# Optimization experiments

Measured on AMD Instinct MI355X. Metric: run time of the kernel, lower is better.

## Reference

```python
import jax, jax.numpy as jnp
import numpy as np

# db4 reconstruction filters (pywt convention): rec_lo = reversed(dec_lo),
# rec_hi[k] = (-1)^k * dec_lo[k]
REC_LO = [0.23037781330885523, 0.7148465705525415, 0.6308807679295904,
          -0.02798376941698385, -0.18703481171888114, 0.030841381835986965,
          0.032883011666982945, -0.010597401784997278]
REC_HI = [-0.010597401784997278, -0.032883011666982945, 0.030841381835986965,
          0.18703481171888114, -0.02798376941698385, -0.6308807679295904,
          0.7148465705525415, -0.23037781330885523]
FILT_LEN = 8


def _idwt1d(cA, cD, axis):
    """Periodized single-level inverse DWT along `axis`. N -> 2N."""
    cA = jnp.moveaxis(cA, axis, -1)
    cD = jnp.moveaxis(cD, axis, -1)
    N = cA.shape[-1]
    up_a = jnp.zeros(cA.shape[:-1] + (2 * N,), cA.dtype).at[..., ::2].set(cA)
    up_d = jnp.zeros(cD.shape[:-1] + (2 * N,), cD.dtype).at[..., ::2].set(cD)
    # circular synthesis: y[m] = sum_k g[k]*up_a[m-k] + h[k]*up_d[m-k]
    y = sum(REC_LO[k] * jnp.roll(up_a, k, axis=-1) +
            REC_HI[k] * jnp.roll(up_d, k, axis=-1) for k in range(FILT_LEN))
    y = jnp.roll(y, -(FILT_LEN - 2), axis=-1)  # phase alignment (periodization)
    return jnp.moveaxis(y, -1, axis)


def setup_inputs() -> dict:
    key = jax.random.key(0)
    x = jax.random.normal(key, (64, 256, 256, 16), dtype=jnp.float32)
    return {"x": x}


def reference(x):
    # x: [B, H, W, 4*C] with channel groups = (cA, cH, cV, cD)
    c = x.shape[-1] // 4
    cA, cH, cV, cD = (x[..., :c], x[..., c:2 * c],
                      x[..., 2 * c:3 * c], x[..., 3 * c:])
    lo = _idwt1d(cA, cH, axis=1)   # [B, 2H, W, C]
    hi = _idwt1d(cV, cD, axis=1)   # [B, 2H, W, C]
    return _idwt1d(lo, hi, axis=2)  # [B, 2H, 2W, C]
```

## Files before the change

### kernel.cpp

```cpp
#include <hip/hip_runtime.h>
#include <hip/hip_bf16.h>


#define N 256
#define RJ 8

typedef float f32x4 __attribute__((ext_vector_type(4)));

#define LGKM_BARRIER()                                   \
  do {                                                   \
    asm volatile("s_waitcnt lgkmcnt(0)" ::: "memory");   \
    __builtin_amdgcn_s_barrier();                        \
    asm volatile("" ::: "memory");                       \
  } while (0)

__device__ __forceinline__ f32x4 fma4v(const f32x4 acc, const float s,
                                       const f32x4 a) {
  const f32x4 sv = {s, s, s, s};
  return __builtin_elementwise_fma(a, sv, acc);
}

__device__ __forceinline__ uint2 pack_bf16x4(const f32x4 v) {
  __hip_bfloat162 lo = __float22bfloat162_rn(make_float2(v.x, v.y));
  __hip_bfloat162 hi = __float22bfloat162_rn(make_float2(v.z, v.w));
  uint2 r;
  r.x = *reinterpret_cast<const unsigned int*>(&lo);
  r.y = *reinterpret_cast<const unsigned int*>(&hi);
  return r;
}

__device__ __forceinline__ f32x4 unpack_bf16x4(const uint2 u) {
  f32x4 r;
  r.x = __uint_as_float(u.x << 16);
  r.y = __uint_as_float(u.x & 0xffff0000u);
  r.z = __uint_as_float(u.y << 16);
  r.w = __uint_as_float(u.y & 0xffff0000u);
  return r;
}

__global__ __launch_bounds__(512, 4) void idwt2_sep12_kernel(
    const float* __restrict__ x, float* __restrict__ out) {
  constexpr float LO[8] = {
      0.23037781330885523f,  0.7148465705525415f,  0.6308807679295904f,
      -0.02798376941698385f, -0.18703481171888114f, 0.030841381835986965f,
      0.032883011666982945f, -0.010597401784997278f};
  constexpr float HIW[8] = {
      -0.010597401784997278f, -0.032883011666982945f, 0.030841381835986965f,
      0.18703481171888114f,  -0.02798376941698385f,  -0.6308807679295904f,
      0.7148465705525415f,   -0.23037781330885523f};
  const float Lw[2][4] = {{LO[6], LO[4], LO[2], LO[0]},
                          {LO[7], LO[5], LO[3], LO[1]}};
  const float Hw[2][4] = {{HIW[6], HIW[4], HIW[2], HIW[0]},
                          {HIW[7], HIW[5], HIW[3], HIW[1]}};

  __shared__ uint2 I[2][2][2][N];

  const int t = threadIdx.x;
  const int bx = blockIdx.x;
  const int b = bx >> 5;
  const int r0 = (bx & 31) * RJ;

  const f32x4* xb = reinterpret_cast<const f32x4*>(x) + (size_t)b * N * N * 4;
  f32x4* ob = reinterpret_cast<f32x4*>(out) + (size_t)b * (2 * N) * (2 * N);

  const int tcol = t & (N - 1);
  const int thalf = t >> 8;
  const f32x4* xcolp = xb + (size_t)tcol * 4 + thalf * 2;

  f32x4 wA[4], wB[4], nA, nB;
  auto ldrow = [&](int lr, f32x4& A, f32x4& B) {
    const int gr = (r0 + lr) & (N - 1);
    A = xcolp[(size_t)gr * (N * 4)];
    B = xcolp[(size_t)gr * (N * 4) + 1];
  };

  auto p1 = [&](int j, int buf) {
    f32x4 v0 = {0.f, 0.f, 0.f, 0.f};
    f32x4 v1 = {0.f, 0.f, 0.f, 0.f};
#pragma unroll
    for (int sy = 0; sy < 4; ++sy) {
      const f32x4 a = wA[(j + sy) & 3];
      const f32x4 bb = wB[(j + sy) & 3];
      v0 = fma4v(v0, Lw[0][sy], a);
      v0 = fma4v(v0, Hw[0][sy], bb);
      v1 = fma4v(v1, Lw[1][sy], a);
      v1 = fma4v(v1, Hw[1][sy], bb);
    }
    I[buf][0][thalf][tcol] = pack_bf16x4(v0);
    I[buf][1][thalf][tcol] = pack_bf16x4(v1);
  };

#pragma unroll
  for (int m = 0; m < 4; ++m) ldrow(m, wA[m], wB[m]);
  ldrow(4, nA, nB);
  p1(0, 0);
  wA[0] = nA;
  wB[0] = nB;
  ldrow(5, nA, nB);
  LGKM_BARRIER();

  const int jx = t >> 1;
  const int q = t & 1;
  float Lq[4], Hq[4];
#pragma unroll
  for (int s = 0; s < 4; ++s) {
    Lq[s] = q ? Lw[1][s] : Lw[0][s];
    Hq[s] = q ? Hw[1][s] : Hw[0][s];
  }

#pragma unroll
  for (int c = 0; c < RJ; ++c) {
    const int buf = c & 1;

    f32x4 o0 = {0.f, 0.f, 0.f, 0.f};
    f32x4 o1 = {0.f, 0.f, 0.f, 0.f};
#pragma unroll
    for (int s = 0; s < 4; ++s) {
      const int xc = (jx + s) & (N - 1);
      const f32x4 l0 = unpack_bf16x4(I[buf][0][0][xc]);
      const f32x4 h0 = unpack_bf16x4(I[buf][0][1][xc]);
      const f32x4 l1 = unpack_bf16x4(I[buf][1][0][xc]);
      const f32x4 h1 = unpack_bf16x4(I[buf][1][1][xc]);
      o0 = fma4v(o0, Lq[s], l0);
      o0 = fma4v(o0, Hq[s], h0);
      o1 = fma4v(o1, Lq[s], l1);
      o1 = fma4v(o1, Hq[s], h1);
    }
    const int jy = r0 + c;
    f32x4* po = ob + (size_t)(2 * jy) * (2 * N) + t;
    po[0] = o0;
    po[2 * N] = o1;

    if (c < RJ - 1) {
      p1(c + 1, buf ^ 1);
      if (c <= RJ - 3) {
        wA[(c + 1) & 3] = nA;
        wB[(c + 1) & 3] = nB;
      }
      if (c <= RJ - 4) ldrow(c + 6, nA, nB);
      LGKM_BARRIER();
    }
  }
}

extern "C" void kernel_launch(void* const* d_in, const int* in_sizes, int n_in,
                              void* d_out, int out_size, void* d_ws,
                              size_t ws_size, hipStream_t stream) {
  const float* x = reinterpret_cast<const float*>(d_in[0]);
  float* out = reinterpret_cast<float*>(d_out);
  const int grid = 64 * (N / RJ);
  idwt2_sep12_kernel<<<grid, 512, 0, stream>>>(x, out);
}
```

Baseline: 122.6 us.

## Double rows per block, deepen prefetch, keep fp32 LDS and bf16 register window

Each block now processes 16 output row pairs instead of 8, reducing the redundant halo rows read per block. The intermediate stored in shared memory switches from packed bf16 to fp32, while the vertical input window in registers is packed to bf16. Global row prefetch is deepened to three rows ahead. This doubles LDS usage per block and halves the grid, which may reduce occupancy and parallelism.

After: 116.1 us. 1.06x faster.

```diff
diff --git a/kernel.cpp b/kernel.cpp
--- a/kernel.cpp
+++ b/kernel.cpp
@@ -3,7 +3,7 @@
 
 
 #define N 256
-#define RJ 8
+#define RJ 16
 
 typedef float f32x4 __attribute__((ext_vector_type(4)));
 
@@ -38,7 +38,7 @@
   return r;
 }
 
-__global__ __launch_bounds__(512, 4) void idwt2_sep12_kernel(
+__global__ __launch_bounds__(512, 4) void idwt2_sep13_kernel(
     const float* __restrict__ x, float* __restrict__ out) {
   constexpr float LO[8] = {
       0.23037781330885523f,  0.7148465705525415f,  0.6308807679295904f,
@@ -53,12 +53,12 @@
   const float Hw[2][4] = {{HIW[6], HIW[4], HIW[2], HIW[0]},
                           {HIW[7], HIW[5], HIW[3], HIW[1]}};
 
-  __shared__ uint2 I[2][2][2][N];
+  __shared__ f32x4 I[2][2][2][N];
 
   const int t = threadIdx.x;
   const int bx = blockIdx.x;
-  const int b = bx >> 5;
-  const int r0 = (bx & 31) * RJ;
+  const int b = bx >> 4;
+  const int r0 = (bx & 15) * RJ;
 
   const f32x4* xb = reinterpret_cast<const f32x4*>(x) + (size_t)b * N * N * 4;
   f32x4* ob = reinterpret_cast<f32x4*>(out) + (size_t)b * (2 * N) * (2 * N);
@@ -67,7 +67,9 @@
   const int thalf = t >> 8;
   const f32x4* xcolp = xb + (size_t)tcol * 4 + thalf * 2;
 
-  f32x4 wA[4], wB[4], nA, nB;
+  uint2 wPA[4], wPB[4];
+  f32x4 pfA[3], pfB[3];
+
   auto ldrow = [&](int lr, f32x4& A, f32x4& B) {
     const int gr = (r0 + lr) & (N - 1);
     A = xcolp[(size_t)gr * (N * 4)];
@@ -79,24 +81,34 @@
     f32x4 v1 = {0.f, 0.f, 0.f, 0.f};
 #pragma unroll
     for (int sy = 0; sy < 4; ++sy) {
-      const f32x4 a = wA[(j + sy) & 3];
-      const f32x4 bb = wB[(j + sy) & 3];
+      const f32x4 a = unpack_bf16x4(wPA[(j + sy) & 3]);
+      const f32x4 bb = unpack_bf16x4(wPB[(j + sy) & 3]);
       v0 = fma4v(v0, Lw[0][sy], a);
       v0 = fma4v(v0, Hw[0][sy], bb);
       v1 = fma4v(v1, Lw[1][sy], a);
       v1 = fma4v(v1, Hw[1][sy], bb);
     }
-    I[buf][0][thalf][tcol] = pack_bf16x4(v0);
-    I[buf][1][thalf][tcol] = pack_bf16x4(v1);
+    I[buf][0][thalf][tcol] = v0;
+    I[buf][1][thalf][tcol] = v1;
   };
 
 #pragma unroll
-  for (int m = 0; m < 4; ++m) ldrow(m, wA[m], wB[m]);
-  ldrow(4, nA, nB);
-  p1(0, 0);
-  wA[0] = nA;
-  wB[0] = nB;
-  ldrow(5, nA, nB);
+  for (int m = 0; m < 4; ++m) {
+    f32x4 A, B;
+    ldrow(m, A, B);
+    wPA[m] = pack_bf16x4(A);
+    wPB[m] = pack_bf16x4(B);
+  }
+  {
+    f32x4 A, B;
+    ldrow(4, A, B);
+    p1(0, 0);
+    wPA[0] = pack_bf16x4(A);
+    wPB[0] = pack_bf16x4(B);
+  }
+  ldrow(5, pfA[2], pfB[2]);
+  ldrow(6, pfA[0], pfB[0]);
+  ldrow(7, pfA[1], pfB[1]);
   LGKM_BARRIER();
 
   const int jx = t >> 1;
@@ -117,14 +129,10 @@
 #pragma unroll
     for (int s = 0; s < 4; ++s) {
       const int xc = (jx + s) & (N - 1);
-      const f32x4 l0 = unpack_bf16x4(I[buf][0][0][xc]);
-      const f32x4 h0 = unpack_bf16x4(I[buf][0][1][xc]);
-      const f32x4 l1 = unpack_bf16x4(I[buf][1][0][xc]);
-      const f32x4 h1 = unpack_bf16x4(I[buf][1][1][xc]);
-      o0 = fma4v(o0, Lq[s], l0);
-      o0 = fma4v(o0, Hq[s], h0);
-      o1 = fma4v(o1, Lq[s], l1);
-      o1 = fma4v(o1, Hq[s], h1);
+      o0 = fma4v(o0, Lq[s], I[buf][0][0][xc]);
+      o0 = fma4v(o0, Hq[s], I[buf][0][1][xc]);
+      o1 = fma4v(o1, Lq[s], I[buf][1][0][xc]);
+      o1 = fma4v(o1, Hq[s], I[buf][1][1][xc]);
     }
     const int jy = r0 + c;
     f32x4* po = ob + (size_t)(2 * jy) * (2 * N) + t;
@@ -134,10 +142,14 @@
     if (c < RJ - 1) {
       p1(c + 1, buf ^ 1);
       if (c <= RJ - 3) {
-        wA[(c + 1) & 3] = nA;
-        wB[(c + 1) & 3] = nB;
+        const int ps = (c + 5) % 3;
+        wPA[(c + 1) & 3] = pack_bf16x4(pfA[ps]);
+        wPB[(c + 1) & 3] = pack_bf16x4(pfB[ps]);
       }
-      if (c <= RJ - 4) ldrow(c + 6, nA, nB);
+      if (c <= RJ - 6) {
+        const int is = (c + 8) % 3;
+        ldrow(c + 8, pfA[is], pfB[is]);
+      }
       LGKM_BARRIER();
     }
   }
@@ -149,5 +161,5 @@
   const float* x = reinterpret_cast<const float*>(d_in[0]);
   float* out = reinterpret_cast<float*>(d_out);
   const int grid = 64 * (N / RJ);
-  idwt2_sep12_kernel<<<grid, 512, 0, stream>>>(x, out);
+  idwt2_sep13_kernel<<<grid, 512, 0, stream>>>(x, out);
 }
```

## Tile columns into 64-wide chunks with halo and keep fp32 intermediates

Applied to the files above, without the earlier changes.

Splits each row block into four 64-column tiles with a 3-column halo and doubles the rows per block to 16, using 256-thread blocks. The bf16 pack/unpack of the vertical-pass intermediate is replaced by fp32 storage in shared memory. Each thread now writes a single output row instead of two. This removes the bf16 precision loss and the conversion work, but adds halo recomputation and idle threads in the first pass.

After: 449.9 us. +267.1%, slower.

```diff
diff --git a/kernel.cpp b/kernel.cpp
--- a/kernel.cpp
+++ b/kernel.cpp
@@ -1,9 +1,10 @@
 #include <hip/hip_runtime.h>
-#include <hip/hip_bf16.h>
 
 
 #define N 256
-#define RJ 8
+#define RJ 16
+#define W 64
+#define HC (W + 3)
 
 typedef float f32x4 __attribute__((ext_vector_type(4)));
 
@@ -20,25 +21,7 @@
   return __builtin_elementwise_fma(a, sv, acc);
 }
 
-__device__ __forceinline__ uint2 pack_bf16x4(const f32x4 v) {
-  __hip_bfloat162 lo = __float22bfloat162_rn(make_float2(v.x, v.y));
-  __hip_bfloat162 hi = __float22bfloat162_rn(make_float2(v.z, v.w));
-  uint2 r;
-  r.x = *reinterpret_cast<const unsigned int*>(&lo);
-  r.y = *reinterpret_cast<const unsigned int*>(&hi);
-  return r;
-}
-
-__device__ __forceinline__ f32x4 unpack_bf16x4(const uint2 u) {
-  f32x4 r;
-  r.x = __uint_as_float(u.x << 16);
-  r.y = __uint_as_float(u.x & 0xffff0000u);
-  r.z = __uint_as_float(u.y << 16);
-  r.w = __uint_as_float(u.y & 0xffff0000u);
-  return r;
-}
-
-__global__ __launch_bounds__(512, 4) void idwt2_sep12_kernel(
+__global__ __launch_bounds__(256, 8) void idwt2_sep15_kernel(
     const float* __restrict__ x, float* __restrict__ out) {
   constexpr float LO[8] = {
       0.23037781330885523f,  0.7148465705525415f,  0.6308807679295904f,
@@ -53,25 +36,31 @@
   const float Hw[2][4] = {{HIW[6], HIW[4], HIW[2], HIW[0]},
                           {HIW[7], HIW[5], HIW[3], HIW[1]}};
 
-  __shared__ uint2 I[2][2][2][N];
+  __shared__ f32x4 I[2][4][HC];
 
   const int t = threadIdx.x;
   const int bx = blockIdx.x;
-  const int b = bx >> 5;
-  const int r0 = (bx & 31) * RJ;
+  const int cq = bx & 3;
+  const int rg = (bx >> 2) & 15;
+  const int b = bx >> 6;
+  const int r0 = rg * RJ;
+  const int jc0 = cq * W;
 
-  const f32x4* xb = reinterpret_cast<const f32x4*>(x) + (size_t)b * N * N * 4;
+  const f32x4* xb4 = reinterpret_cast<const f32x4*>(x) + (size_t)b * N * N * 4;
   f32x4* ob = reinterpret_cast<f32x4*>(out) + (size_t)b * (2 * N) * (2 * N);
 
-  const int tcol = t & (N - 1);
-  const int thalf = t >> 8;
-  const f32x4* xcolp = xb + (size_t)tcol * 4 + thalf * 2;
+  const bool doP1 = t < 2 * HC;
+  const int c_ = t >> 1;
+  const int sh = t & 1;
+  const int scol = (jc0 + c_) & (N - 1);
+  const f32x4* xcolp = xb4 + (size_t)scol * 4 + sh * 2;
 
   f32x4 wA[4], wB[4], nA, nB;
   auto ldrow = [&](int lr, f32x4& A, f32x4& B) {
     const int gr = (r0 + lr) & (N - 1);
-    A = xcolp[(size_t)gr * (N * 4)];
-    B = xcolp[(size_t)gr * (N * 4) + 1];
+    const f32x4* p = xcolp + (size_t)gr * (N * 4);
+    A = p[0];
+    B = p[1];
   };
 
   auto p1 = [&](int j, int buf) {
@@ -86,21 +75,25 @@
       v1 = fma4v(v1, Lw[1][sy], a);
       v1 = fma4v(v1, Hw[1][sy], bb);
     }
-    I[buf][0][thalf][tcol] = pack_bf16x4(v0);
-    I[buf][1][thalf][tcol] = pack_bf16x4(v1);
+    I[buf][2 * sh + 0][c_] = v0;
+    I[buf][2 * sh + 1][c_] = v1;
   };
 
+  if (doP1) {
 #pragma unroll
-  for (int m = 0; m < 4; ++m) ldrow(m, wA[m], wB[m]);
-  ldrow(4, nA, nB);
-  p1(0, 0);
-  wA[0] = nA;
-  wB[0] = nB;
-  ldrow(5, nA, nB);
+    for (int m = 0; m < 4; ++m) ldrow(m, wA[m], wB[m]);
+    ldrow(4, nA, nB);
+    p1(0, 0);
+    wA[0] = nA;
+    wB[0] = nB;
+    ldrow(5, nA, nB);
+  }
   LGKM_BARRIER();
 
-  const int jx = t >> 1;
-  const int q = t & 1;
+  const int pp = t >> 7;
+  const int colf4 = t & 127;
+  const int jx = colf4 >> 1;
+  const int q = colf4 & 1;
   float Lq[4], Hq[4];
 #pragma unroll
   for (int s = 0; s < 4; ++s) {
@@ -112,32 +105,25 @@
   for (int c = 0; c < RJ; ++c) {
     const int buf = c & 1;
 
-    f32x4 o0 = {0.f, 0.f, 0.f, 0.f};
-    f32x4 o1 = {0.f, 0.f, 0.f, 0.f};
+    f32x4 o = {0.f, 0.f, 0.f, 0.f};
 #pragma unroll
     for (int s = 0; s < 4; ++s) {
-      const int xc = (jx + s) & (N - 1);
-      const f32x4 l0 = unpack_bf16x4(I[buf][0][0][xc]);
-      const f32x4 h0 = unpack_bf16x4(I[buf][0][1][xc]);
-      const f32x4 l1 = unpack_bf16x4(I[buf][1][0][xc]);
-      const f32x4 h1 = unpack_bf16x4(I[buf][1][1][xc]);
-      o0 = fma4v(o0, Lq[s], l0);
-      o0 = fma4v(o0, Hq[s], h0);
-      o1 = fma4v(o1, Lq[s], l1);
-      o1 = fma4v(o1, Hq[s], h1);
+      const int xc = jx + s;
+      o = fma4v(o, Lq[s], I[buf][pp][xc]);
+      o = fma4v(o, Hq[s], I[buf][2 + pp][xc]);
     }
     const int jy = r0 + c;
-    f32x4* po = ob + (size_t)(2 * jy) * (2 * N) + t;
-    po[0] = o0;
-    po[2 * N] = o1;
+    ob[(size_t)(2 * jy + pp) * (2 * N) + 2 * jc0 + colf4] = o;
 
     if (c < RJ - 1) {
-      p1(c + 1, buf ^ 1);
-      if (c <= RJ - 3) {
-        wA[(c + 1) & 3] = nA;
-        wB[(c + 1) & 3] = nB;
+      if (doP1) {
+        p1(c + 1, buf ^ 1);
+        if (c <= RJ - 3) {
+          wA[(c + 1) & 3] = nA;
+          wB[(c + 1) & 3] = nB;
+        }
+        if (c <= RJ - 4) ldrow(c + 6, nA, nB);
       }
-      if (c <= RJ - 4) ldrow(c + 6, nA, nB);
       LGKM_BARRIER();
     }
   }
@@ -148,6 +134,6 @@
                               size_t ws_size, hipStream_t stream) {
   const float* x = reinterpret_cast<const float*>(d_in[0]);
   float* out = reinterpret_cast<float*>(d_out);
-  const int grid = 64 * (N / RJ);
-  idwt2_sep12_kernel<<<grid, 512, 0, stream>>>(x, out);
+  const int grid = 64 * (N / RJ) * (N / W);
+  idwt2_sep15_kernel<<<grid, 256, 0, stream>>>(x, out);
 }
```
